# Optimization experiments

Hardware: AMD Instinct MI355X
Metric: run time of the kernel (lower is better)

Reference implementation:

```python
import jax, jax.numpy as jnp
import numpy as np

B, TY, ENC, EMB, DEC, V = 16, 255, 512, 256, 512, 32000
EPS = 1e-5


def _lstm(x, Wih, Whh, bih, bhh):
    # x: [B, T, Din]; torch gate order i, f, g, o; h0 = c0 = 0
    Bb = x.shape[0]
    H = Whh.shape[1]
    xw = jnp.einsum('btd,gd->btg', x, Wih) + bih + bhh  # [B, T, 4H]

    def step(carry, xt):
        h, c = carry
        g = xt + h @ Whh.T
        i, f, gg, o = jnp.split(g, 4, axis=-1)
        i = jax.nn.sigmoid(i)
        f = jax.nn.sigmoid(f)
        gg = jnp.tanh(gg)
        o = jax.nn.sigmoid(o)
        c = f * c + i * gg
        h = o * jnp.tanh(c)
        return (h, c), h

    h0 = jnp.zeros((Bb, H), x.dtype)
    _, hs = jax.lax.scan(step, (h0, h0), jnp.swapaxes(xw, 0, 1))
    return jnp.swapaxes(hs, 0, 1)  # [B, T, H]


def setup_inputs():
    key = jax.random.key(0)
    ks = jax.random.split(key, 16)
    s = 0.05
    rn = lambda k, sh: jax.random.normal(k, sh, jnp.float32)
    return {
        'x': rn(ks[0], (B, ENC)),
        'y': jax.random.randint(ks[1], (B, TY), 0, V),
        'fc1_w': rn(ks[2], (EMB, ENC)) * s,
        'fc1_b': rn(ks[3], (EMB,)) * s,
        'bn_g': jnp.ones((EMB,), jnp.float32),
        'bn_b': jnp.zeros((EMB,), jnp.float32),
        'emb': rn(ks[4], (V, EMB)) * s,
        'l1_Wih': rn(ks[5], (4 * DEC, EMB)) * s,
        'l1_Whh': rn(ks[6], (4 * DEC, DEC)) * s,
        'l1_bih': rn(ks[7], (4 * DEC,)) * s,
        'l1_bhh': rn(ks[8], (4 * DEC,)) * s,
        'attn_Wout': rn(ks[9], (DEC, 2 * DEC)) * s,
        'dc_Wih': rn(ks[10], (4 * DEC, DEC)) * s,
        'dc_Whh': rn(ks[11], (4 * DEC, DEC)) * s,
        'dc_bih': rn(ks[12], (4 * DEC,)) * s,
        'dc_bhh': rn(ks[13], (4 * DEC,)) * s,
        'fc2_w': rn(ks[14], (V, DEC)) * s,
        'fc2_b': rn(ks[15], (V,)) * s,
        'lengths': TY + 1,  # all sequences full length
    }


def reference(x, y, fc1_w, fc1_b, bn_g, bn_b, emb, l1_Wih, l1_Whh, l1_bih, l1_bhh,
              attn_Wout, dc_Wih, dc_Whh, dc_bih, dc_bhh, fc2_w, fc2_b, lengths):
    # fc1 + BatchNorm1d (training-mode batch stats, biased var)
    feat = x @ fc1_w.T + fc1_b                         # [B, EMB]
    mu = feat.mean(axis=0)
    var = feat.var(axis=0)
    feat = (feat - mu) / jnp.sqrt(var + EPS) * bn_g + bn_b
    # prepend feature to embedded tokens -> [B, L, EMB], L = TY + 1
    seq = jnp.concatenate([feat[:, None, :], emb[y]], axis=1)
    # first LSTM
    h = _lstm(seq, l1_Wih, l1_Whh, l1_bih, l1_bhh)     # [B, L, DEC]
    L = seq.shape[1]
    # causal dot-product self-attention (vectorized form of the python loop)
    scores = jnp.einsum('bqd,bkd->bqk', h, h)
    mask = jnp.tril(jnp.ones((L, L), bool))
    w = jax.nn.softmax(jnp.where(mask, scores, -1e30), axis=-1)
    mix = jnp.einsum('bqk,bkd->bqd', w, h)
    attn = jnp.tanh(jnp.concatenate([mix, h], axis=-1) @ attn_Wout.T)
    # decoder LSTM cell over attended features
    out = _lstm(attn, dc_Wih, dc_Whh, dc_bih, dc_bhh)  # [B, L, DEC]
    return out @ fc2_w.T + fc2_b                       # [B, L, V]
```

## Files before the change

kernel.cpp:

```cpp
#include <hip/hip_runtime.h>

#define BB 16
#define TY 255
#define ENC 512
#define EMBD 256
#define DEC 512
#define VV 32000
#define LL 256
#define M4 4096
#define GG 2048
#define SENT 0x7FC0

typedef unsigned short u16;
typedef __attribute__((ext_vector_type(8))) short short8;
typedef __attribute__((ext_vector_type(4))) float f32x4;
typedef __attribute__((ext_vector_type(4))) unsigned short u16x4;

__device__ __forceinline__ u16 f2bf(float f) {
  unsigned u = __float_as_uint(f);
  u += 0x7fff + ((u >> 16) & 1);
  return (u16)(u >> 16);
}
__device__ __forceinline__ f32x4 mfma16(short8 a, short8 b, f32x4 c) {
  return __builtin_amdgcn_mfma_f32_16x16x32_bf16(a, b, c, 0, 0, 0);
}
__device__ __forceinline__ float fsig(float x) { return 1.f / (1.f + __expf(-x)); }
__device__ __forceinline__ float ftanh(float x) { return 2.f / (1.f + __expf(-2.f * x)) - 1.f; }

__device__ __forceinline__ void st_b32_dev(int* a, int v) {
  asm volatile("global_store_dword %0, %1, off sc1" :: "v"(a), "v"(v) : "memory");
}
__device__ __forceinline__ void gload_lds16(const u16* g, u16* l) {
  __builtin_amdgcn_global_load_lds(
      (const __attribute__((address_space(1))) void*)g,
      (__attribute__((address_space(3))) void*)l, 16, 0, 0);
}

template<bool BT, bool OBF, bool DOTANH, bool BIAS>
__global__ __launch_bounds__(256) void gemm_kernel(
    const u16* __restrict__ A, const u16* __restrict__ Bm, void* __restrict__ Cv,
    const float* __restrict__ bias,
    int K, int lda, int ldb, int ldc,
    long a_bs, long b_bs, long c_bs)
{
  __shared__ u16 As[64][72];
  __shared__ u16 Bs[64][72];
  const int tid = threadIdx.x;
  const long m0 = (long)blockIdx.y * 64, n0 = (long)blockIdx.x * 64;
  const int z = blockIdx.z;
  const u16* Ab = A + (long)z * a_bs;
  const u16* Bb = Bm + (long)z * b_bs;
  const int lane = tid & 63, w = tid >> 6;
  const int wm = w >> 1, wn = w & 1;
  f32x4 acc[2][2] = {};
  for (int k0 = 0; k0 < K; k0 += 64) {
#pragma unroll
    for (int i = 0; i < 2; i++) {
      int c = tid + 256 * i;
      int r = c >> 3, kk = (c & 7) << 3;
      *(short8*)&As[r][kk] = *(const short8*)&Ab[(m0 + r) * (long)lda + k0 + kk];
    }
    if (BT) {
#pragma unroll
      for (int i = 0; i < 2; i++) {
        int c = tid + 256 * i;
        int r = c >> 3, kk = (c & 7) << 3;
        *(short8*)&Bs[r][kk] = *(const short8*)&Bb[(n0 + r) * (long)ldb + k0 + kk];
      }
    } else {
#pragma unroll
      for (int i = 0; i < 2; i++) {
        int c = tid + 256 * i;
        int kk = c >> 3, nn = (c & 7) << 3;
        const u16* s = &Bb[(long)(k0 + kk) * ldb + n0 + nn];
#pragma unroll
        for (int j = 0; j < 8; j++) Bs[nn + j][kk] = s[j];
      }
    }
    __syncthreads();
#pragma unroll
    for (int kf = 0; kf < 2; kf++) {
      const int ko = kf * 32 + (lane >> 4) * 8;
      short8 a0 = *(const short8*)&As[wm * 32 + (lane & 15)][ko];
      short8 a1 = *(const short8*)&As[wm * 32 + 16 + (lane & 15)][ko];
      short8 b0 = *(const short8*)&Bs[wn * 32 + (lane & 15)][ko];
      short8 b1 = *(const short8*)&Bs[wn * 32 + 16 + (lane & 15)][ko];
      acc[0][0] = mfma16(a0, b0, acc[0][0]);
      acc[0][1] = mfma16(a0, b1, acc[0][1]);
      acc[1][0] = mfma16(a1, b0, acc[1][0]);
      acc[1][1] = mfma16(a1, b1, acc[1][1]);
    }
    __syncthreads();
  }
#pragma unroll
  for (int m = 0; m < 2; m++)
#pragma unroll
    for (int n = 0; n < 2; n++) {
#pragma unroll
      for (int r = 0; r < 4; r++) {
        long row = m0 + wm * 32 + m * 16 + (lane >> 4) * 4 + r;
        long col = n0 + wn * 32 + n * 16 + (lane & 15);
        float v = acc[m][n][r];
        if (BIAS) v += bias[col];
        if (DOTANH) v = tanhf(v);
        if (OBF) ((u16*)Cv)[(long)z * c_bs + row * ldc + col] = f2bf(v);
        else ((float*)Cv)[(long)z * c_bs + row * ldc + col] = v;
      }
    }
}

template<bool OBF, bool DOTANH, bool BIAS>
__global__ __launch_bounds__(256) void gemm128_kernel(
    const u16* __restrict__ A, const u16* __restrict__ Bm, void* __restrict__ Cv,
    const float* __restrict__ bias,
    int K, int lda, int ldb, int ldc,
    long a_bs, long b_bs, long c_bs)
{
  __shared__ u16 As[128 * 64];
  __shared__ u16 Bs[128 * 64];
  const int tid = threadIdx.x;
  const long m0 = (long)blockIdx.y * 128, n0 = (long)blockIdx.x * 128;
  const int z = blockIdx.z;
  const u16* Ab = A + (long)z * a_bs;
  const u16* Bb = Bm + (long)z * b_bs;
  const int lane = tid & 63, w = tid >> 6;
  const int wm = w >> 1, wn = w & 1;
  const int rr = tid >> 3, kk = (tid & 7) << 3;
  f32x4 acc[4][4] = {};
  for (int k0 = 0; k0 < K; k0 += 64) {
#pragma unroll
    for (int i = 0; i < 4; i++) {
      gload_lds16(&Ab[(m0 + i * 32 + rr) * (long)lda + k0 + kk],
                  As + (i * 256 + (w << 6)) * 8);
      gload_lds16(&Bb[(n0 + i * 32 + rr) * (long)ldb + k0 + kk],
                  Bs + (i * 256 + (w << 6)) * 8);
    }
    __syncthreads();
#pragma unroll
    for (int kf = 0; kf < 2; kf++) {
      const int ko = kf * 32 + (lane >> 4) * 8;
      short8 a[4], b[4];
#pragma unroll
      for (int mi = 0; mi < 4; mi++)
        a[mi] = *(const short8*)&As[(wm * 64 + mi * 16 + (lane & 15)) * 64 + ko];
#pragma unroll
      for (int ni = 0; ni < 4; ni++)
        b[ni] = *(const short8*)&Bs[(wn * 64 + ni * 16 + (lane & 15)) * 64 + ko];
#pragma unroll
      for (int mi = 0; mi < 4; mi++)
#pragma unroll
        for (int ni = 0; ni < 4; ni++)
          acc[mi][ni] = mfma16(a[mi], b[ni], acc[mi][ni]);
    }
    __syncthreads();
  }
#pragma unroll
  for (int mi = 0; mi < 4; mi++)
#pragma unroll
    for (int ni = 0; ni < 4; ni++) {
#pragma unroll
      for (int r = 0; r < 4; r++) {
        long row = m0 + wm * 64 + mi * 16 + (lane >> 4) * 4 + r;
        long col = n0 + wn * 64 + ni * 16 + (lane & 15);
        float v = acc[mi][ni][r];
        if (BIAS) v += bias[col];
        if (DOTANH) v = tanhf(v);
        if (OBF) ((u16*)Cv)[(long)z * c_bs + row * ldc + col] = f2bf(v);
        else ((float*)Cv)[(long)z * c_bs + row * ldc + col] = v;
      }
    }
}

__global__ void sentinel_kernel(u16* __restrict__ p) {
  long i = ((long)blockIdx.x * 256 + threadIdx.x) * 8;
  short v = (i < 8192) ? (short)0 : (short)SENT;
  short8 s = {v, v, v, v, v, v, v, v};
  *(short8*)&p[i] = s;
}

template<int MODE>
__global__ __launch_bounds__(256) void lstm_kernel(
    const float* __restrict__ xw,
    const u16* __restrict__ Whh,
    u16* __restrict__ Hseq,
    u16* __restrict__ hout)
{
  const int nb = blockIdx.x;
  const int tid = threadIdx.x;
  const int lane = tid & 63, w = tid >> 6;
  __shared__ u16 hs[16][520];
  __shared__ float gbuf[16][64];
  const int ncol0 = nb * 64 + w * 16;
  short8 bfrag[16];
  {
    const u16* wr = Whh + (long)(ncol0 + (lane & 15)) * 512 + ((lane >> 4) * 8);
#pragma unroll
    for (int kf = 0; kf < 16; kf++) bfrag[kf] = *(const short8*)&wr[kf * 32];
  }
  const int b = tid >> 4, jl = tid & 15;
  const int jglob = nb * 16 + jl;
  int cc[4];
#pragma unroll
  for (int i = 0; i < 4; i++) cc[i] = (tid + i * 256 + nb * 32) & 1023;
  float c = 0.f;
  float4 xg = *(const float4*)&xw[((long)b * LL) * GG + nb * 64 + jl * 4];
  for (int t = 0; t < LL; t++) {
    const u16* Hin = Hseq + (long)t * 8192;
    short8 svA[4], svB[4];
#pragma unroll
    for (int i = 0; i < 4; i++)
      asm volatile("global_load_dwordx4 %0, %1, off sc1"
                   : "=v"(svA[i]) : "v"(Hin + (cc[i] >> 6) * 512 + (cc[i] & 63) * 8));
    for (;;) {
#pragma unroll
      for (int i = 0; i < 4; i++)
        asm volatile("global_load_dwordx4 %0, %1, off sc1"
                     : "=v"(svB[i]) : "v"(Hin + (cc[i] >> 6) * 512 + (cc[i] & 63) * 8));
      asm volatile("s_waitcnt vmcnt(4)" ::: "memory");
      __builtin_amdgcn_sched_barrier(0);
      {
        int bad = 0;
#pragma unroll
        for (int i = 0; i < 4; i++) {
          const int* dv = (const int*)&svA[i];
#pragma unroll
          for (int d = 0; d < 4; d++) bad |= ((dv[d] & 0xFFFF) == SENT);
        }
        if (!__any(bad)) {
#pragma unroll
          for (int i = 0; i < 4; i++)
            *(short8*)&hs[cc[i] >> 6][(cc[i] & 63) * 8] = svA[i];
          break;
        }
      }
#pragma unroll
      for (int i = 0; i < 4; i++)
        asm volatile("global_load_dwordx4 %0, %1, off sc1"
                     : "=v"(svA[i]) : "v"(Hin + (cc[i] >> 6) * 512 + (cc[i] & 63) * 8));
      asm volatile("s_waitcnt vmcnt(4)" ::: "memory");
      __builtin_amdgcn_sched_barrier(0);
      {
        int bad = 0;
#pragma unroll
        for (int i = 0; i < 4; i++) {
          const int* dv = (const int*)&svB[i];
#pragma unroll
          for (int d = 0; d < 4; d++) bad |= ((dv[d] & 0xFFFF) == SENT);
        }
        if (!__any(bad)) {
#pragma unroll
          for (int i = 0; i < 4; i++)
            *(short8*)&hs[cc[i] >> 6][(cc[i] & 63) * 8] = svB[i];
          break;
        }
      }
    }
    asm volatile("s_waitcnt vmcnt(0)" ::: "memory");
    __syncthreads();
    f32x4 acc0 = {}, acc1 = {};
#pragma unroll
    for (int kf = 0; kf < 8; kf++) {
      short8 a0 = *(const short8*)&hs[lane & 15][(lane >> 4) * 8 + (2 * kf) * 32];
      short8 a1 = *(const short8*)&hs[lane & 15][(lane >> 4) * 8 + (2 * kf + 1) * 32];
      acc0 = mfma16(a0, bfrag[2 * kf], acc0);
      acc1 = mfma16(a1, bfrag[2 * kf + 1], acc1);
    }
    f32x4 acc = acc0 + acc1;
#pragma unroll
    for (int r = 0; r < 4; r++)
      gbuf[(lane >> 4) * 4 + r][w * 16 + (lane & 15)] = acc[r];
    __syncthreads();
    float gi = fsig(gbuf[b][jl * 4 + 0] + xg.x);
    float gf = fsig(gbuf[b][jl * 4 + 1] + xg.y);
    float gg = ftanh(gbuf[b][jl * 4 + 2] + xg.z);
    float go = fsig(gbuf[b][jl * 4 + 3] + xg.w);
    c = gf * c + gi * gg;
    float h = go * ftanh(c);
    u16 hb = f2bf(h);
    unsigned hi16 = (unsigned)__shfl_down((int)(unsigned)hb, 1);
    if ((jl & 1) == 0) {
      int pk = (int)((unsigned)hb | (hi16 << 16));
      st_b32_dev((int*)&Hseq[((long)t + 1) * 8192 + b * 512 + jglob], pk);
    }
    if (MODE == 0) hout[((long)b * LL + t) * 1024 + 512 + jglob] = hb;
    else           hout[((long)b * LL + t) * 512 + jglob] = hb;
    if (t + 1 < LL)
      xg = *(const float4*)&xw[((long)b * LL + (t + 1)) * GG + nb * 64 + jl * 4];
  }
}

__global__ void fc1_kernel(const float* __restrict__ x, const float* __restrict__ wgt,
                           const float* __restrict__ bias, float* __restrict__ feat) {
  __shared__ float xs[ENC];
  int bb = blockIdx.x, j = threadIdx.x;
  for (int k = j; k < ENC; k += 256) xs[k] = x[bb * ENC + k];
  __syncthreads();
  float s = bias[j];
  const float* wr = wgt + (long)j * ENC;
  for (int k = 0; k < ENC; k += 4) {
    float4 wv = *(const float4*)&wr[k];
    s += xs[k] * wv.x + xs[k + 1] * wv.y + xs[k + 2] * wv.z + xs[k + 3] * wv.w;
  }
  feat[bb * EMBD + j] = s;
}

__global__ void bn_embed0_kernel(const float* __restrict__ feat, const float* __restrict__ g,
                                 const float* __restrict__ bb, u16* __restrict__ seq) {
  int j = threadIdx.x;
  float mu = 0.f, m2 = 0.f;
  for (int i = 0; i < BB; i++) { float v = feat[i * EMBD + j]; mu += v; m2 += v * v; }
  mu *= (1.f / BB);
  float var = m2 * (1.f / BB) - mu * mu;
  float sc = g[j] * rsqrtf(var + 1e-5f);
  float sh = bb[j];
  for (int i = 0; i < BB; i++) {
    float v = (feat[i * EMBD + j] - mu) * sc + sh;
    seq[((long)i * LL) * EMBD + j] = f2bf(v);
  }
}

__global__ void embed_kernel(const int* __restrict__ y, const float* __restrict__ emb,
                             u16* __restrict__ seq) {
  int t = blockIdx.x, bb = blockIdx.y;
  int tok = y[bb * TY + t];
  int j = threadIdx.x;
  seq[((long)bb * LL + 1 + t) * EMBD + j] = f2bf(emb[(long)tok * EMBD + j]);
}

__global__ __launch_bounds__(256) void softmax_kernel(const float* __restrict__ sc,
                                                      u16* __restrict__ wsm) {
  int row = blockIdx.x;
  int q = row & (LL - 1);
  int k = threadIdx.x;
  __shared__ float red[8];
  float v = (k <= q) ? sc[(long)row * LL + k] : -3.4e38f;
  float m = v;
#pragma unroll
  for (int o = 32; o > 0; o >>= 1) m = fmaxf(m, __shfl_xor(m, o));
  if ((k & 63) == 0) red[k >> 6] = m;
  __syncthreads();
  m = fmaxf(fmaxf(red[0], red[1]), fmaxf(red[2], red[3]));
  float e = (k <= q) ? expf(v - m) : 0.f;
  float s = e;
#pragma unroll
  for (int o = 32; o > 0; o >>= 1) s += __shfl_xor(s, o);
  if ((k & 63) == 0) red[4 + (k >> 6)] = s;
  __syncthreads();
  s = red[4] + red[5] + red[6] + red[7];
  wsm[(long)row * LL + k] = f2bf(e / s);
}

__global__ void conv_bf16_kernel(const float* __restrict__ s, u16* __restrict__ d) {
  long i = ((long)blockIdx.x * 256 + threadIdx.x) * 4;
  float4 v = *(const float4*)&s[i];
  u16x4 o = {f2bf(v.x), f2bf(v.y), f2bf(v.z), f2bf(v.w)};
  *(u16x4*)&d[i] = o;
}

__global__ void conv_lstm_w_kernel(const float* __restrict__ s, u16* __restrict__ d, int ldk) {
  int n = blockIdx.x;
  int r = (n & 3) * DEC + (n >> 2);
  for (int k = threadIdx.x; k < ldk; k += 256)
    d[(long)n * ldk + k] = f2bf(s[(long)r * ldk + k]);
}

__global__ void conv_lstm_b_kernel(const float* __restrict__ bih, const float* __restrict__ bhh,
                                   float* __restrict__ d) {
  int n = blockIdx.x * 256 + threadIdx.x;
  int r = (n & 3) * DEC + (n >> 2);
  d[n] = bih[r] + bhh[r];
}

extern "C" void kernel_launch(void* const* d_in, const int* in_sizes, int n_in,
                              void* d_out, int out_size, void* d_ws, size_t ws_size,
                              hipStream_t stream) {
  const float* x      = (const float*)d_in[0];
  const int*   y      = (const int*)d_in[1];
  const float* fc1_w  = (const float*)d_in[2];
  const float* fc1_b  = (const float*)d_in[3];
  const float* bn_g   = (const float*)d_in[4];
  const float* bn_b   = (const float*)d_in[5];
  const float* emb    = (const float*)d_in[6];
  const float* l1_Wih = (const float*)d_in[7];
  const float* l1_Whh = (const float*)d_in[8];
  const float* l1_bih = (const float*)d_in[9];
  const float* l1_bhh = (const float*)d_in[10];
  const float* Wout   = (const float*)d_in[11];
  const float* dc_Wih = (const float*)d_in[12];
  const float* dc_Whh = (const float*)d_in[13];
  const float* dc_bih = (const float*)d_in[14];
  const float* dc_bhh = (const float*)d_in[15];
  const float* fc2_w  = (const float*)d_in[16];
  const float* fc2_b  = (const float*)d_in[17];
  float* out = (float*)d_out;

  char* ws = (char*)d_ws;
  float* xw     = (float*)(ws + 0);
  u16*   seqb   = (u16*)(ws + 33554432);
  u16*   cat    = (u16*)(ws + 35651584);
  float* scores = (float*)(ws + 44040192);
  u16*   Hseq   = (u16*)(ws + 44040192);
  u16*   wsm    = (u16*)(ws + 48234496);
  u16*   attnb  = (u16*)(ws + 50331648);
  u16*   h2b    = (u16*)(ws + 54525952);
  u16*   wih1   = (u16*)(ws + 58720256);
  u16*   whh1   = (u16*)(ws + 59768832);
  u16*   wih2   = (u16*)(ws + 61865984);
  u16*   whh2   = (u16*)(ws + 63963136);
  u16*   woutb  = (u16*)(ws + 66060288);
  u16*   fc2wb  = (u16*)(ws + 67108864);
  float* b1p    = (float*)(ws + 99876864);
  float* b2p    = (float*)(ws + 99885056);
  float* feat   = (float*)(ws + 99893248);

  conv_lstm_w_kernel<<<GG, 256, 0, stream>>>(l1_Wih, wih1, EMBD);
  conv_lstm_w_kernel<<<GG, 256, 0, stream>>>(l1_Whh, whh1, DEC);
  conv_lstm_w_kernel<<<GG, 256, 0, stream>>>(dc_Wih, wih2, DEC);
  conv_lstm_w_kernel<<<GG, 256, 0, stream>>>(dc_Whh, whh2, DEC);
  conv_lstm_b_kernel<<<GG / 256, 256, 0, stream>>>(l1_bih, l1_bhh, b1p);
  conv_lstm_b_kernel<<<GG / 256, 256, 0, stream>>>(dc_bih, dc_bhh, b2p);
  conv_bf16_kernel<<<(DEC * 2 * DEC) / 1024, 256, 0, stream>>>(Wout, woutb);
  conv_bf16_kernel<<<(VV * DEC) / 1024, 256, 0, stream>>>(fc2_w, fc2wb);

  fc1_kernel<<<BB, 256, 0, stream>>>(x, fc1_w, fc1_b, feat);
  bn_embed0_kernel<<<1, 256, 0, stream>>>(feat, bn_g, bn_b, seqb);
  embed_kernel<<<dim3(TY, BB), 256, 0, stream>>>(y, emb, seqb);

  gemm128_kernel<false, false, true><<<dim3(GG / 128, M4 / 128, 1), 256, 0, stream>>>(
      seqb, wih1, xw, b1p, EMBD, EMBD, EMBD, GG, 0, 0, 0);
  sentinel_kernel<<<1028, 256, 0, stream>>>(Hseq);
  lstm_kernel<0><<<32, 256, 0, stream>>>(xw, whh1, Hseq, cat);
  gemm128_kernel<false, false, false><<<dim3(LL / 128, LL / 128, BB), 256, 0, stream>>>(
      cat + 512, cat + 512, scores, nullptr, DEC, 1024, 1024, LL,
      (long)LL * 1024, (long)LL * 1024, (long)LL * LL);
  softmax_kernel<<<M4, 256, 0, stream>>>(scores, wsm);
  gemm_kernel<false, true, false, false><<<dim3(DEC / 64, LL / 64, BB), 256, 0, stream>>>(
      wsm, cat + 512, cat, nullptr, LL, LL, 1024, 1024,
      (long)LL * LL, (long)LL * 1024, (long)LL * 1024);
  gemm128_kernel<true, true, false><<<dim3(DEC / 128, M4 / 128, 1), 256, 0, stream>>>(
      cat, woutb, attnb, nullptr, 1024, 1024, 1024, DEC, 0, 0, 0);
  gemm128_kernel<false, false, true><<<dim3(GG / 128, M4 / 128, 1), 256, 0, stream>>>(
      attnb, wih2, xw, b2p, DEC, DEC, DEC, GG, 0, 0, 0);
  sentinel_kernel<<<1028, 256, 0, stream>>>(Hseq);
  lstm_kernel<1><<<32, 256, 0, stream>>>(xw, whh2, Hseq, h2b);
  gemm128_kernel<false, false, true><<<dim3(VV / 128, M4 / 128, 1), 256, 0, stream>>>(
      h2b, fc2wb, out, fc2_b, DEC, DEC, DEC, VV, 0, 0, 0);
}
```

Measured before the change: 1.487 ms.

## Run recurrent LSTM kernels on 8 blocks of 1024 threads instead of 32x256

The persistent LSTM recurrence kernels now run on 8 workgroups of 1024 threads rather than 32 of 256. Each block owns 256 gate columns (64 hidden units), and each thread polls and copies one 16-byte chunk of the previous h instead of four. Fewer blocks means fewer participants in the cross-block spin-wait on the sentinel-marked h buffer each timestep, and less redundant polling traffic. The cost is that only 8 CUs are used and each CU carries a heavier per-step MFMA, activation and synchronisation load, with larger workgroup-wide barriers.

```diff
diff --git a/kernel.cpp b/kernel.cpp
--- a/kernel.cpp
+++ b/kernel.cpp
@@ -179,7 +179,7 @@
 }
 
 template<int MODE>
-__global__ __launch_bounds__(256) void lstm_kernel(
+__global__ __launch_bounds__(1024) void lstm_kernel(
     const float* __restrict__ xw,
     const u16* __restrict__ Whh,
     u16* __restrict__ Hseq,
@@ -189,70 +189,44 @@
   const int tid = threadIdx.x;
   const int lane = tid & 63, w = tid >> 6;
   __shared__ u16 hs[16][520];
-  __shared__ float gbuf[16][64];
-  const int ncol0 = nb * 64 + w * 16;
+  __shared__ float gbuf[16][256];
+  const int ncol0 = nb * 256 + w * 16;
   short8 bfrag[16];
   {
     const u16* wr = Whh + (long)(ncol0 + (lane & 15)) * 512 + ((lane >> 4) * 8);
 #pragma unroll
     for (int kf = 0; kf < 16; kf++) bfrag[kf] = *(const short8*)&wr[kf * 32];
   }
-  const int b = tid >> 4, jl = tid & 15;
-  const int jglob = nb * 16 + jl;
-  int cc[4];
-#pragma unroll
-  for (int i = 0; i < 4; i++) cc[i] = (tid + i * 256 + nb * 32) & 1023;
+  const int b = tid >> 6, jl = tid & 63;
+  const int jglob = nb * 64 + jl;
+  const int cc = (tid + nb * 128) & 1023;
+  const int coff = (cc >> 6) * 512 + (cc & 63) * 8;
   float c = 0.f;
-  float4 xg = *(const float4*)&xw[((long)b * LL) * GG + nb * 64 + jl * 4];
+  float4 xg = *(const float4*)&xw[((long)b * LL) * GG + nb * 256 + jl * 4];
   for (int t = 0; t < LL; t++) {
-    const u16* Hin = Hseq + (long)t * 8192;
-    short8 svA[4], svB[4];
-#pragma unroll
-    for (int i = 0; i < 4; i++)
-      asm volatile("global_load_dwordx4 %0, %1, off sc1"
-                   : "=v"(svA[i]) : "v"(Hin + (cc[i] >> 6) * 512 + (cc[i] & 63) * 8));
+    const u16* ap = Hseq + (long)t * 8192 + coff;
+    short8 svA, svB;
+    asm volatile("global_load_dwordx4 %0, %1, off sc1" : "=v"(svA) : "v"(ap));
     for (;;) {
-#pragma unroll
-      for (int i = 0; i < 4; i++)
-        asm volatile("global_load_dwordx4 %0, %1, off sc1"
-                     : "=v"(svB[i]) : "v"(Hin + (cc[i] >> 6) * 512 + (cc[i] & 63) * 8));
-      asm volatile("s_waitcnt vmcnt(4)" ::: "memory");
+      asm volatile("global_load_dwordx4 %0, %1, off sc1" : "=v"(svB) : "v"(ap));
+      asm volatile("s_waitcnt vmcnt(1)" ::: "memory");
       __builtin_amdgcn_sched_barrier(0);
       {
+        const int* dv = (const int*)&svA;
         int bad = 0;
 #pragma unroll
-        for (int i = 0; i < 4; i++) {
-          const int* dv = (const int*)&svA[i];
-#pragma unroll
-          for (int d = 0; d < 4; d++) bad |= ((dv[d] & 0xFFFF) == SENT);
-        }
-        if (!__any(bad)) {
-#pragma unroll
-          for (int i = 0; i < 4; i++)
-            *(short8*)&hs[cc[i] >> 6][(cc[i] & 63) * 8] = svA[i];
-          break;
-        }
-      }
-#pragma unroll
-      for (int i = 0; i < 4; i++)
-        asm volatile("global_load_dwordx4 %0, %1, off sc1"
-                     : "=v"(svA[i]) : "v"(Hin + (cc[i] >> 6) * 512 + (cc[i] & 63) * 8));
-      asm volatile("s_waitcnt vmcnt(4)" ::: "memory");
+        for (int d = 0; d < 4; d++) bad |= ((dv[d] & 0xFFFF) == SENT);
+        if (!__any(bad)) { *(short8*)&hs[cc >> 6][(cc & 63) * 8] = svA; break; }
+      }
+      asm volatile("global_load_dwordx4 %0, %1, off sc1" : "=v"(svA) : "v"(ap));
+      asm volatile("s_waitcnt vmcnt(1)" ::: "memory");
       __builtin_amdgcn_sched_barrier(0);
       {
+        const int* dv = (const int*)&svB;
         int bad = 0;
 #pragma unroll
-        for (int i = 0; i < 4; i++) {
-          const int* dv = (const int*)&svB[i];
-#pragma unroll
-          for (int d = 0; d < 4; d++) bad |= ((dv[d] & 0xFFFF) == SENT);
-        }
-        if (!__any(bad)) {
-#pragma unroll
-          for (int i = 0; i < 4; i++)
-            *(short8*)&hs[cc[i] >> 6][(cc[i] & 63) * 8] = svB[i];
-          break;
-        }
+        for (int d = 0; d < 4; d++) bad |= ((dv[d] & 0xFFFF) == SENT);
+        if (!__any(bad)) { *(short8*)&hs[cc >> 6][(cc & 63) * 8] = svB; break; }
       }
     }
     asm volatile("s_waitcnt vmcnt(0)" ::: "memory");
@@ -285,7 +259,7 @@
     if (MODE == 0) hout[((long)b * LL + t) * 1024 + 512 + jglob] = hb;
     else           hout[((long)b * LL + t) * 512 + jglob] = hb;
     if (t + 1 < LL)
-      xg = *(const float4*)&xw[((long)b * LL + (t + 1)) * GG + nb * 64 + jl * 4];
+      xg = *(const float4*)&xw[((long)b * LL + (t + 1)) * GG + nb * 256 + jl * 4];
   }
 }
 
@@ -429,7 +403,7 @@
   gemm128_kernel<false, false, true><<<dim3(GG / 128, M4 / 128, 1), 256, 0, stream>>>(
       seqb, wih1, xw, b1p, EMBD, EMBD, EMBD, GG, 0, 0, 0);
   sentinel_kernel<<<1028, 256, 0, stream>>>(Hseq);
-  lstm_kernel<0><<<32, 256, 0, stream>>>(xw, whh1, Hseq, cat);
+  lstm_kernel<0><<<8, 1024, 0, stream>>>(xw, whh1, Hseq, cat);
   gemm128_kernel<false, false, false><<<dim3(LL / 128, LL / 128, BB), 256, 0, stream>>>(
       cat + 512, cat + 512, scores, nullptr, DEC, 1024, 1024, LL,
       (long)LL * 1024, (long)LL * 1024, (long)LL * LL);
@@ -442,7 +416,7 @@
   gemm128_kernel<false, false, true><<<dim3(GG / 128, M4 / 128, 1), 256, 0, stream>>>(
       attnb, wih2, xw, b2p, DEC, DEC, DEC, GG, 0, 0, 0);
   sentinel_kernel<<<1028, 256, 0, stream>>>(Hseq);
-  lstm_kernel<1><<<32, 256, 0, stream>>>(xw, whh2, Hseq, h2b);
+  lstm_kernel<1><<<8, 1024, 0, stream>>>(xw, whh2, Hseq, h2b);
   gemm128_kernel<false, false, true><<<dim3(VV / 128, M4 / 128, 1), 256, 0, stream>>>(
       h2b, fc2wb, out, fc2_b, DEC, DEC, DEC, VV, 0, 0, 0);
 }
```

Result: slower. 2.303 ms (+54.8%).
